# Kernel tuning notes

Hardware: AMD Instinct MI355X
Metric: run time of the kernel (lower is better)

Reference implementation:

```python
import jax, jax.numpy as jnp
import numpy as np

C = 10.0
EMBEDDING_DIM = 128


def setup_inputs() -> dict:
    key = jax.random.key(0)
    k1, k2 = jax.random.split(key)
    B, P, D, N = 128, 128, 128, 4096
    mh_attn_out = jax.random.normal(k1, (B, P, D), dtype=jnp.float32)
    single_head_key = jax.random.normal(k2, (B, D, N), dtype=jnp.float32)
    mask = jnp.zeros((B, P, N), dtype=jnp.float32)  # additive mask (0 or -inf)
    return {"mh_attn_out": mh_attn_out, "single_head_key": single_head_key, "mask": mask}


def reference(mh_attn_out, single_head_key, mask):
    # score: [B, P, N]
    score = jnp.einsum('bpd,bdn->bpn', mh_attn_out, single_head_key)
    score_scaled = score / jnp.sqrt(jnp.float32(EMBEDDING_DIM))
    score_clipped = C * jnp.tanh(score_scaled)
    score_masked = score_clipped + mask
    probs = jax.nn.softmax(score_masked, axis=-1)
    return probs
```

## Files before the change

### kernel.cpp

```cpp
#include <hip/hip_runtime.h>
#include <math.h>

constexpr int BB = 128;
constexpr int PP = 128;
constexpr int DD = 128;
constexpr int NN = 4096;
constexpr float kC = 10.0f;
constexpr float k2InvSqrtD = 0.1767766952966369f;

constexpr int NTHR = 512;
constexpr int TEL = 272;

typedef float f32x4 __attribute__((ext_vector_type(4)));
typedef _Float16 f16x4 __attribute__((ext_vector_type(4)));
typedef _Float16 f16x8 __attribute__((ext_vector_type(8)));

__device__ __forceinline__ void st_nt_f4(float* p, float4 s) {
    f32x4 v = {s.x, s.y, s.z, s.w};
    __builtin_nontemporal_store(v, (f32x4*)p);
}

__device__ __forceinline__ f16x4 tr_read(unsigned addr) {
    f16x4 r;
    asm volatile("ds_read_b64_tr_b16 %0, %1" : "=v"(r) : "v"(addr));
    return r;
}

__device__ __forceinline__ float clip1(float s, float m) {
    const float e2 = __expf(s * k2InvSqrtD);
    const float r = __builtin_amdgcn_rcpf(e2 + 1.0f);
    return fmaf(-2.0f * kC, r, kC) + m;
}

__global__ __launch_bounds__(NTHR, 2)
void score_kernel(const float* __restrict__ A,
                  const float* __restrict__ K,
                  const float* __restrict__ M,
                  float* __restrict__ O,
                  float* __restrict__ ws) {
    __shared__ _Float16 Khi[32 * TEL];
    __shared__ _Float16 Klo[32 * TEL];

    const int l = blockIdx.x;
    const int b = l >> 5;
    const int ntb = l & 31;
    const int n_base = ntb * 128;

    const int tid = (int)threadIdx.x;
    const int lane = tid & 63;
    const int wid = tid >> 6;
    const int col = lane & 15;
    const int g = lane >> 4;
    const int kbase = 4 * g;

    const float* Arow = A + (size_t)(b * PP + wid * 16 + col) * DD;
    f16x8 ah[4], al[4];
    #pragma unroll
    for (int kb = 0; kb < 4; ++kb) {
        #pragma unroll
        for (int j = 0; j < 8; ++j) {
            const int d = kb * 32 + kbase + (j & 3) + 16 * (j >> 2);
            const float x = Arow[d];
            const _Float16 h = (_Float16)x;
            ah[kb][j] = h;
            al[kb][j] = (_Float16)(x - (float)h);
        }
    }

    const size_t mrow0 = (size_t)(b * PP + wid * 16 + kbase) * NN + n_base + col;
    const unsigned khi0 = (unsigned)(uintptr_t)&Khi[0] + (unsigned)lane * 8u;
    const unsigned klo0 = (unsigned)(uintptr_t)&Klo[0] + (unsigned)lane * 8u;

    const float* Kg = K + (size_t)b * DD * NN + n_base;
    const int nl4 = (tid & 15) * 4;
    const int d0 = tid >> 4;
    const int ntile = nl4 >> 4;
    const int nin = nl4 & 12;

    float rsum[4] = {0.f, 0.f, 0.f, 0.f};

    float mv[4];
    #pragma unroll
    for (int j = 0; j < 4; ++j) mv[j] = M[mrow0 + (size_t)j * NN];

    #pragma unroll
    for (int half = 0; half < 2; ++half) {
        if (half) __syncthreads();

        #pragma unroll
        for (int i = 0; i < 4; ++i) {
            const int d = d0 + 32 * i;
            const float4 v = *(const float4*)(Kg + (size_t)d * NN + half * 64 + nl4);
            const float xs[4] = {v.x, v.y, v.z, v.w};
            f16x4 h, lo;
            #pragma unroll
            for (int e = 0; e < 4; ++e) {
                const _Float16 hh = (_Float16)xs[e];
                h[e] = hh;
                lo[e] = (_Float16)(xs[e] - (float)hh);
            }
            const int el = ((d >> 4) * 4 + ntile) * TEL + (d & 15) * 16 + nin;
            *(f16x4*)&Khi[el] = h;
            *(f16x4*)&Klo[el] = lo;
        }
        __syncthreads();

        #pragma unroll
        for (int nt2 = 0; nt2 < 4; ++nt2) {
            const int nt = half * 4 + nt2;

            float mvn[4] = {0.f, 0.f, 0.f, 0.f};
            if (nt < 7) {
                #pragma unroll
                for (int j = 0; j < 4; ++j)
                    mvn[j] = M[mrow0 + (size_t)j * NN + (nt + 1) * 16];
            }

            f16x4 bh0[4], bh1[4], bl0[4], bl1[4];
            #pragma unroll
            for (int kb = 0; kb < 4; ++kb) {
                const unsigned t0 = (unsigned)(((2 * kb) * 4 + nt2) * 544);
                bh0[kb] = tr_read(khi0 + t0);
                bh1[kb] = tr_read(khi0 + t0 + 4u * 544u);
                bl0[kb] = tr_read(klo0 + t0);
                bl1[kb] = tr_read(klo0 + t0 + 4u * 544u);
            }
            asm volatile("s_waitcnt lgkmcnt(0)" ::: "memory");
            __builtin_amdgcn_sched_barrier(0);

            f32x4 acc = {0.f, 0.f, 0.f, 0.f};
            #pragma unroll
            for (int kb = 0; kb < 4; ++kb) {
                const f16x8 bh = __builtin_shufflevector(bh0[kb], bh1[kb], 0, 1, 2, 3, 4, 5, 6, 7);
                const f16x8 bl = __builtin_shufflevector(bl0[kb], bl1[kb], 0, 1, 2, 3, 4, 5, 6, 7);
                acc = __builtin_amdgcn_mfma_f32_16x16x32_f16(ah[kb], bh, acc, 0, 0, 0);
                acc = __builtin_amdgcn_mfma_f32_16x16x32_f16(ah[kb], bl, acc, 0, 0, 0);
                acc = __builtin_amdgcn_mfma_f32_16x16x32_f16(al[kb], bh, acc, 0, 0, 0);
            }

            #pragma unroll
            for (int j = 0; j < 4; ++j) {
                const size_t off = mrow0 + (size_t)j * NN + nt * 16;
                const float e = __expf(clip1(acc[j], mv[j]));
                O[off] = e;
                rsum[j] += e;
            }
            #pragma unroll
            for (int j = 0; j < 4; ++j) mv[j] = mvn[j];
        }
    }

    #pragma unroll
    for (int j = 0; j < 4; ++j) {
        float s = rsum[j];
        s += __shfl_xor(s, 1);
        s += __shfl_xor(s, 2);
        s += __shfl_xor(s, 4);
        s += __shfl_xor(s, 8);
        rsum[j] = s;
    }
    if (col == 0) {
        #pragma unroll
        for (int j = 0; j < 4; ++j)
            ws[(size_t)(b * PP + wid * 16 + kbase + j) * 32 + ntb] = rsum[j];
    }
}

__global__ __launch_bounds__(256, 4)
void scale_kernel(float* __restrict__ O, const float* __restrict__ ws) {
    const int gtid = blockIdx.x * 256 + (int)threadIdx.x;
    const int row = gtid >> 5;
    const int seg = gtid & 31;

    const float* w = ws + (size_t)row * 32;
    float s = 0.f;
    #pragma unroll
    for (int i = 0; i < 8; ++i) {
        const float4 v = *(const float4*)(w + i * 4);
        s += (v.x + v.y) + (v.z + v.w);
    }
    const float inv = __builtin_amdgcn_rcpf(s);

    float4* R = (float4*)(O + (size_t)row * NN);
    #pragma unroll 8
    for (int i = 0; i < 32; ++i) {
        const int idx = i * 32 + seg;
        float4 v = R[idx];
        v.x *= inv; v.y *= inv; v.z *= inv; v.w *= inv;
        st_nt_f4((float*)&R[idx], v);
    }
}

extern "C" void kernel_launch(void* const* d_in, const int* in_sizes, int n_in,
                              void* d_out, int out_size, void* d_ws, size_t ws_size,
                              hipStream_t stream) {
    const float* A = (const float*)d_in[0];
    const float* K = (const float*)d_in[1];
    const float* M = (const float*)d_in[2];
    float* O = (float*)d_out;
    float* ws = (float*)d_ws;

    score_kernel<<<dim3(BB * 32), dim3(NTHR), 0, stream>>>(A, K, M, O, ws);
    scale_kernel<<<dim3(2048), dim3(256), 0, stream>>>(O, ws);
}
```

Before: 272.2 us.

## Double-buffer K tiles in LDS and widen each block to 256 columns

Each block now covers 256 N columns instead of 128, halving the grid and the per-block A load and f16 split overhead. K tiles are double-buffered in shared memory: the next tile's global load is issued into registers and split into the alternate buffer while MFMAs run on the current one, and the mask prefetch is deepened to three tiles. Per-row partial sums shrink from 32 to 16 entries. The cost is double the LDS footprint and more live registers, which may reduce occupancy, and fewer blocks across the GPU.

```diff
diff --git a/kernel.cpp b/kernel.cpp
--- a/kernel.cpp
+++ b/kernel.cpp
@@ -38,13 +38,13 @@
                   const float* __restrict__ M,
                   float* __restrict__ O,
                   float* __restrict__ ws) {
-    __shared__ _Float16 Khi[32 * TEL];
-    __shared__ _Float16 Klo[32 * TEL];
+    __shared__ _Float16 Khi[2][32 * TEL];
+    __shared__ _Float16 Klo[2][32 * TEL];
 
     const int l = blockIdx.x;
-    const int b = l >> 5;
-    const int ntb = l & 31;
-    const int n_base = ntb * 128;
+    const int b = l >> 4;
+    const int ntb = l & 15;
+    const int n_base = ntb * 256;
 
     const int tid = (int)threadIdx.x;
     const int lane = tid & 63;
@@ -68,30 +68,26 @@
     }
 
     const size_t mrow0 = (size_t)(b * PP + wid * 16 + kbase) * NN + n_base + col;
-    const unsigned khi0 = (unsigned)(uintptr_t)&Khi[0] + (unsigned)lane * 8u;
-    const unsigned klo0 = (unsigned)(uintptr_t)&Klo[0] + (unsigned)lane * 8u;
+    const unsigned khiB = (unsigned)(uintptr_t)&Khi[0][0] + (unsigned)lane * 8u;
+    const unsigned kloB = (unsigned)(uintptr_t)&Klo[0][0] + (unsigned)lane * 8u;
+    const unsigned BUFB = (unsigned)(32 * TEL * 2);
 
     const float* Kg = K + (size_t)b * DD * NN + n_base;
     const int nl4 = (tid & 15) * 4;
     const int d0 = tid >> 4;
     const int ntile = nl4 >> 4;
     const int nin = nl4 & 12;
-
-    float rsum[4] = {0.f, 0.f, 0.f, 0.f};
-
-    float mv[4];
-    #pragma unroll
-    for (int j = 0; j < 4; ++j) mv[j] = M[mrow0 + (size_t)j * NN];
-
-    #pragma unroll
-    for (int half = 0; half < 2; ++half) {
-        if (half) __syncthreads();
-
+    const int el0 = ((d0 >> 4) * 4 + ntile) * TEL + (d0 & 15) * 16 + nin;
+
+    auto loadK = [&](int q, float4* kr) {
+        #pragma unroll
+        for (int i = 0; i < 4; ++i)
+            kr[i] = *(const float4*)(Kg + (size_t)(d0 + 32 * i) * NN + q * 64 + nl4);
+    };
+    auto splitK = [&](const float4* kr, int nb) {
         #pragma unroll
         for (int i = 0; i < 4; ++i) {
-            const int d = d0 + 32 * i;
-            const float4 v = *(const float4*)(Kg + (size_t)d * NN + half * 64 + nl4);
-            const float xs[4] = {v.x, v.y, v.z, v.w};
+            const float xs[4] = {kr[i].x, kr[i].y, kr[i].z, kr[i].w};
             f16x4 h, lo;
             #pragma unroll
             for (int e = 0; e < 4; ++e) {
@@ -99,22 +95,36 @@
                 h[e] = hh;
                 lo[e] = (_Float16)(xs[e] - (float)hh);
             }
-            const int el = ((d >> 4) * 4 + ntile) * TEL + (d & 15) * 16 + nin;
-            *(f16x4*)&Khi[el] = h;
-            *(f16x4*)&Klo[el] = lo;
+            const int el = el0 + i * 8 * TEL;
+            *(f16x4*)&Khi[nb][el] = h;
+            *(f16x4*)&Klo[nb][el] = lo;
         }
-        __syncthreads();
+    };
+
+    float rsum[4] = {0.f, 0.f, 0.f, 0.f};
+
+    float4 kreg[4];
+    loadK(0, kreg);
+    splitK(kreg, 0);
+    loadK(1, kreg);
+
+    float mva[4], mvb[4], mvc[4];
+    #pragma unroll
+    for (int j = 0; j < 4; ++j) mva[j] = M[mrow0 + (size_t)j * NN + 0 * 16];
+    #pragma unroll
+    for (int j = 0; j < 4; ++j) mvb[j] = M[mrow0 + (size_t)j * NN + 1 * 16];
+    #pragma unroll
+    for (int j = 0; j < 4; ++j) mvc[j] = M[mrow0 + (size_t)j * NN + 2 * 16];
+    __syncthreads();
+
+    #pragma unroll
+    for (int h = 0; h < 4; ++h) {
+        const unsigned khi0 = khiB + (unsigned)(h & 1) * BUFB;
+        const unsigned klo0 = kloB + (unsigned)(h & 1) * BUFB;
 
         #pragma unroll
         for (int nt2 = 0; nt2 < 4; ++nt2) {
-            const int nt = half * 4 + nt2;
-
-            float mvn[4] = {0.f, 0.f, 0.f, 0.f};
-            if (nt < 7) {
-                #pragma unroll
-                for (int j = 0; j < 4; ++j)
-                    mvn[j] = M[mrow0 + (size_t)j * NN + (nt + 1) * 16];
-            }
+            const int nt = h * 4 + nt2;
 
             f16x4 bh0[4], bh1[4], bl0[4], bl1[4];
             #pragma unroll
@@ -141,13 +151,25 @@
             #pragma unroll
             for (int j = 0; j < 4; ++j) {
                 const size_t off = mrow0 + (size_t)j * NN + nt * 16;
-                const float e = __expf(clip1(acc[j], mv[j]));
+                const float e = __expf(clip1(acc[j], mva[j]));
                 O[off] = e;
                 rsum[j] += e;
             }
-            #pragma unroll
-            for (int j = 0; j < 4; ++j) mv[j] = mvn[j];
+
+            #pragma unroll
+            for (int j = 0; j < 4; ++j) { mva[j] = mvb[j]; mvb[j] = mvc[j]; }
+            if (nt + 3 < 16) {
+                #pragma unroll
+                for (int j = 0; j < 4; ++j)
+                    mvc[j] = M[mrow0 + (size_t)j * NN + (nt + 3) * 16];
+            }
+
+            if (nt2 == 0) {
+                if (h < 3) splitK(kreg, (h + 1) & 1);
+                if (h < 2) loadK(h + 2, kreg);
+            }
         }
+        if (h < 3) __syncthreads();
     }
 
     #pragma unroll
@@ -162,7 +184,7 @@
     if (col == 0) {
         #pragma unroll
         for (int j = 0; j < 4; ++j)
-            ws[(size_t)(b * PP + wid * 16 + kbase + j) * 32 + ntb] = rsum[j];
+            ws[(size_t)(b * PP + wid * 16 + kbase + j) * 16 + ntb] = rsum[j];
     }
 }
 
@@ -172,10 +194,10 @@
     const int row = gtid >> 5;
     const int seg = gtid & 31;
 
-    const float* w = ws + (size_t)row * 32;
+    const float* w = ws + (size_t)row * 16;
     float s = 0.f;
     #pragma unroll
-    for (int i = 0; i < 8; ++i) {
+    for (int i = 0; i < 4; ++i) {
         const float4 v = *(const float4*)(w + i * 4);
         s += (v.x + v.y) + (v.z + v.w);
     }
@@ -200,6 +222,6 @@
     float* O = (float*)d_out;
     float* ws = (float*)d_ws;
 
-    score_kernel<<<dim3(BB * 32), dim3(NTHR), 0, stream>>>(A, K, M, O, ws);
+    score_kernel<<<dim3(BB * 16), dim3(NTHR), 0, stream>>>(A, K, M, O, ws);
     scale_kernel<<<dim3(2048), dim3(256), 0, stream>>>(O, ws);
 }
```

New measurement: 285.7 us. 1.05x slower.
